# Optimization experiments

Hardware: AMD Instinct MI355X
Metric: run time of the kernel (lower is better)

The kernel has to match this reference:

```python
import jax, jax.numpy as jnp
import numpy as np

B, T, C, H, W = 2, 1, 256, 64, 64
K = 16384  # codebook_size

def setup_inputs() -> dict:
    key = jax.random.key(0)
    k1, k2 = jax.random.split(key)
    x = jax.random.normal(k1, (B, T, C, H, W), dtype=jnp.float32)
    # original init: uniform(-1/K, 1/K); scale is irrelevant for argmin correctness
    codebook = jax.random.uniform(k2, (K, C), dtype=jnp.float32,
                                  minval=-1.0 / K, maxval=1.0 / K)
    return {"x": x, "codebook": codebook}

def reference(x, codebook):
    b, t, c, h, w = x.shape
    # (b,t,c,h,w) -> (b,t,h,w,c) -> (N, c)
    xf = jnp.transpose(x, (0, 1, 3, 4, 2)).reshape(-1, c)
    x_sq = jnp.sum(xf * xf, axis=1, keepdims=True)          # (N, 1)
    e_sq = jnp.sum(codebook * codebook, axis=1)             # (K,)
    d = x_sq + e_sq - 2.0 * jnp.einsum('nd,kd->nk', xf, codebook)  # (N, K)
    indices = jnp.argmin(d, axis=1)
    return indices.reshape(b, t, h, w)
```

## Files before the change

### kernel.cpp

```cpp
#include <hip/hip_runtime.h>
#include <hip/hip_bf16.h>
#include <stdint.h>

constexpr int C    = 256;
constexpr int HW   = 4096;
constexpr int NPIX = 8192;
constexpr int K    = 16384;

constexpr int BM = 128;
constexpr int BN = 256;
constexpr int NB = K / BN;
constexpr float DELTA = 1e-4f;
constexpr unsigned PAIR_CAP = 262144;

typedef __attribute__((ext_vector_type(8))) short short8;
typedef __attribute__((ext_vector_type(4))) float f32x4;
typedef unsigned int u32;
typedef unsigned long long u64;

constexpr size_t OFF_KEYS  = 0;
constexpr size_t OFF_XSQ   = 65536;
constexpr size_t OFF_MHAT  = 98304;
constexpr size_t OFF_CNT   = 131072;
constexpr size_t OFF_PAIRS = 131328;
constexpr size_t OFF_MIN1  = 1179904;
constexpr size_t OFF_K1    = 3277056;
constexpr size_t OFF_MIN2  = 5374208;
constexpr size_t OFF_XT    = 7471360;

static __device__ __forceinline__ unsigned short f2bf(float f) {
    __hip_bfloat16 h = __float2bfloat16(f);
    return *reinterpret_cast<unsigned short*>(&h);
}

__global__ __launch_bounds__(256) void vqprep_kernel(
    const float* __restrict__ x,
    float* __restrict__ xsq, u64* __restrict__ keys,
    unsigned* __restrict__ mhat, unsigned* __restrict__ cnt,
    unsigned short* __restrict__ xt)
{
    __shared__ float lds[64][65];
    const int bid = blockIdx.x;
    const int t   = threadIdx.x;
    if (bid < 32) {
        const int p  = bid * 256 + t;
        const int b  = p >> 12;
        const int hw = p & 4095;
        const float* xp = x + (size_t)b * C * HW + hw;
        float acc = 0.0f;
        #pragma unroll 8
        for (int c = 0; c < C; ++c) {
            const float v = xp[(size_t)c * HW];
            acc = fmaf(v, v, acc);
        }
        xsq[p]  = acc;
        keys[p] = ~0ULL;
        mhat[p] = 0x7F7FFFFFu;
        if (p == 0) *cnt = 0u;
    } else {
        const int bid2 = bid - 32;
        const int hw0 = (bid2 & 63) * 64;
        const int c0  = ((bid2 >> 6) & 3) * 64;
        const int b   = bid2 >> 8;
        #pragma unroll
        for (int i = 0; i < 4; ++i) {
            const int ch  = i * 16 + (t >> 4);
            const int pix = (t & 15) * 4;
            const float4 v = *(const float4*)&x[((size_t)(b * C + c0 + ch)) * HW + hw0 + pix];
            lds[ch][pix + 0] = v.x; lds[ch][pix + 1] = v.y;
            lds[ch][pix + 2] = v.z; lds[ch][pix + 3] = v.w;
        }
        __syncthreads();
        #pragma unroll
        for (int j = 0; j < 4; ++j) {
            const int pix = j * 16 + (t >> 4);
            const int cs  = (t & 15) * 4;
            const u32 lo = (u32)f2bf(lds[cs + 0][pix]) | ((u32)f2bf(lds[cs + 1][pix]) << 16);
            const u32 hi = (u32)f2bf(lds[cs + 2][pix]) | ((u32)f2bf(lds[cs + 3][pix]) << 16);
            const int p = b * HW + hw0 + pix;
            *(uint2*)&xt[(size_t)p * C + c0 + cs] = make_uint2(lo, hi);
        }
    }
}

__global__ __launch_bounds__(256, 2) void vqgemm_kernel(
    const unsigned short* __restrict__ xt, const float* __restrict__ cb,
    float* __restrict__ min1a, unsigned* __restrict__ k1a, float* __restrict__ min2a,
    unsigned* __restrict__ mhat)
{
    __shared__ unsigned short a_lds[128 * 64];
    __shared__ unsigned short b_lds[256 * 64];

    const int t    = threadIdx.x;
    const int lane = t & 63;
    const int wid  = t >> 6;
    const int wr   = wid >> 1;
    const int wc   = wid & 1;
    const int p0 = blockIdx.x * BM;
    const int n0 = blockIdx.y * BN;

    f32x4 acc[4][8];
    #pragma unroll
    for (int i = 0; i < 4; ++i)
        #pragma unroll
        for (int j = 0; j < 8; ++j) acc[i][j] = (f32x4){0.f, 0.f, 0.f, 0.f};

    for (int ks = 0; ks < 4; ++ks) {
        __syncthreads();
        {
            const int r = t >> 1, h = t & 1;
            const char* src = (const char*)xt + (size_t)(p0 + r) * 512 + ks * 128 + h * 64;
            #pragma unroll
            for (int j = 0; j < 4; ++j) {
                const uint4 v = *(const uint4*)(src + j * 16);
                const int s = h * 4 + j;
                *(uint4*)&a_lds[r * 64 + (s ^ (r & 7)) * 8] = v;
            }
        }
        {
            #pragma unroll
            for (int R = 0; R < 4; ++R) {
                const int row = R * 64 + (t >> 2);
                const int seg = t & 3;
                const float* src = cb + (size_t)(n0 + row) * C + ks * 64 + seg * 16;
                u32 w[8];
                #pragma unroll
                for (int j = 0; j < 4; ++j) {
                    const float4 v = *(const float4*)(src + j * 4);
                    w[j * 2 + 0] = (u32)f2bf(v.x) | ((u32)f2bf(v.y) << 16);
                    w[j * 2 + 1] = (u32)f2bf(v.z) | ((u32)f2bf(v.w) << 16);
                }
                const int s0 = seg * 2;
                *(uint4*)&b_lds[row * 64 + ((s0 + 0) ^ (row & 7)) * 8] = make_uint4(w[0], w[1], w[2], w[3]);
                *(uint4*)&b_lds[row * 64 + ((s0 + 1) ^ (row & 7)) * 8] = make_uint4(w[4], w[5], w[6], w[7]);
            }
        }
        __syncthreads();
        #pragma unroll
        for (int kk2 = 0; kk2 < 2; ++kk2) {
            short8 af[4], bfq[8];
            const int sl = kk2 * 4 + (lane >> 4);
            #pragma unroll
            for (int mf = 0; mf < 4; ++mf) {
                const int row = wr * 64 + mf * 16 + (lane & 15);
                af[mf] = *(const short8*)&a_lds[row * 64 + (sl ^ (row & 7)) * 8];
            }
            #pragma unroll
            for (int nf = 0; nf < 8; ++nf) {
                const int row = wc * 128 + nf * 16 + (lane & 15);
                bfq[nf] = *(const short8*)&b_lds[row * 64 + (sl ^ (row & 7)) * 8];
            }
            #pragma unroll
            for (int mf = 0; mf < 4; ++mf)
                #pragma unroll
                for (int nf = 0; nf < 8; ++nf)
                    acc[mf][nf] = __builtin_amdgcn_mfma_f32_16x16x32_bf16(af[mf], bfq[nf], acc[mf][nf], 0, 0, 0);
        }
    }

    __syncthreads();
    u32* tri = (u32*)a_lds;

    #pragma unroll
    for (int mf = 0; mf < 4; ++mf) {
        #pragma unroll
        for (int q = 0; q < 4; ++q) {
            float m1 = 3.4e38f, m2 = 3.4e38f; int kl = 0;
            #pragma unroll
            for (int nf = 0; nf < 8; ++nf) {
                const float v = fmaf(-2.0f, acc[mf][nf][q], 4.0f);
                const int kk = wc * 128 + nf * 16 + (lane & 15);
                if (v < m1) { m2 = m1; m1 = v; kl = kk; }
                else        { m2 = fminf(m2, v); }
            }
            for (int s = 1; s < 16; s <<= 1) {
                const float om1 = __shfl_xor(m1, s);
                const float om2 = __shfl_xor(m2, s);
                const int   okl = __shfl_xor(kl, s);
                if (om1 < m1) { m2 = fminf(m1, om2); m1 = om1; kl = okl; }
                else          { m2 = fminf(om1, m2); }
            }
            if ((lane & 15) == 0) {
                const int pixloc = wr * 64 + mf * 16 + (lane >> 4) * 4 + q;
                const int base = (pixloc * 2 + wc) * 3;
                tri[base + 0] = __float_as_uint(m1);
                tri[base + 1] = (u32)kl;
                tri[base + 2] = __float_as_uint(m2);
            }
        }
    }
    __syncthreads();
    if (t < 128) {
        const int b0 = (t * 2 + 0) * 3, b1 = (t * 2 + 1) * 3;
        float m1 = __uint_as_float(tri[b0 + 0]); u32 kl = tri[b0 + 1];
        float m2 = __uint_as_float(tri[b0 + 2]);
        const float om1 = __uint_as_float(tri[b1 + 0]);
        const u32   okl = tri[b1 + 1];
        const float om2 = __uint_as_float(tri[b1 + 2]);
        if (om1 < m1) { m2 = fminf(m1, om2); m1 = om1; kl = okl; }
        else          { m2 = fminf(om1, m2); }
        const int p = p0 + t;
        const size_t idx = (size_t)p * NB + blockIdx.y;
        min1a[idx] = m1;
        k1a[idx]   = (u32)n0 + kl;
        min2a[idx] = m2;
        atomicMin(&mhat[p], __float_as_uint(m1));
    }
}

__global__ __launch_bounds__(256) void vqflag_kernel(
    const float* __restrict__ min1a, const unsigned* __restrict__ k1a,
    const float* __restrict__ min2a, const unsigned* __restrict__ mhat,
    unsigned* __restrict__ cnt, unsigned* __restrict__ pairs)
{
    const int idx = blockIdx.x * 256 + threadIdx.x;
    if (idx >= NPIX * NB) return;
    const int p  = idx >> 6;
    const int nb = idx & 63;
    const float thresh = __uint_as_float(mhat[p]) + DELTA;
    if (min1a[idx] <= thresh) {
        const unsigned pos = atomicAdd(cnt, 1u);
        if (pos < PAIR_CAP) pairs[pos] = ((unsigned)p << 14) | k1a[idx];
    }
    if (min2a[idx] <= thresh) {
        const unsigned base = atomicAdd(cnt, 256u);
        for (int j = 0; j < 256; ++j)
            if (base + j < PAIR_CAP) pairs[base + j] = ((unsigned)p << 14) | (unsigned)(nb * 256 + j);
    }
}

__global__ __launch_bounds__(256) void vqexact_kernel(
    const float* __restrict__ x, const float* __restrict__ cb,
    const float* __restrict__ xsq, const unsigned* __restrict__ cnt,
    const unsigned* __restrict__ pairs, u64* __restrict__ keys)
{
    const unsigned n = min(*cnt, PAIR_CAP);
    for (unsigned i = blockIdx.x * 256 + threadIdx.x; i < n; i += gridDim.x * 256) {
        const unsigned pair = pairs[i];
        const int p = pair >> 14;
        const int k = pair & 16383;
        const int b = p >> 12;
        const int hw = p & 4095;
        const float* xp = x + (size_t)b * C * HW + hw;
        const float* ep = cb + (size_t)k * C;
        float acc = 0.0f;
        #pragma unroll 4
        for (int c = 0; c < C; ++c)
            acc = fmaf(xp[(size_t)c * HW], ep[c], acc);
        const float d = xsq[p] - 2.0f * acc;
        const u64 key = ((u64)__float_as_uint(d) << 32) | (unsigned)k;
        atomicMin(&keys[p], key);
    }
}

__global__ __launch_bounds__(256) void vqout_kernel(
    const u64* __restrict__ keys, int* __restrict__ out)
{
    const int p = blockIdx.x * 256 + threadIdx.x;
    out[p] = (int)(unsigned)(keys[p] & 0xffffffffu);
}

extern "C" void kernel_launch(void* const* d_in, const int* in_sizes, int n_in,
                              void* d_out, int out_size, void* d_ws, size_t ws_size,
                              hipStream_t stream)
{
    const float* x  = (const float*)d_in[0];
    const float* cb = (const float*)d_in[1];
    int* out = (int*)d_out;
    char* ws = (char*)d_ws;

    u64*      keys  = (u64*)(ws + OFF_KEYS);
    float*    xsq   = (float*)(ws + OFF_XSQ);
    unsigned* mhat  = (unsigned*)(ws + OFF_MHAT);
    unsigned* cnt   = (unsigned*)(ws + OFF_CNT);
    unsigned* pairs = (unsigned*)(ws + OFF_PAIRS);
    float*    min1a = (float*)(ws + OFF_MIN1);
    unsigned* k1a   = (unsigned*)(ws + OFF_K1);
    float*    min2a = (float*)(ws + OFF_MIN2);
    unsigned short* xt = (unsigned short*)(ws + OFF_XT);

    vqprep_kernel<<<544, 256, 0, stream>>>(x, xsq, keys, mhat, cnt, xt);
    vqgemm_kernel<<<dim3(NPIX / BM, K / BN), 256, 0, stream>>>(xt, cb, min1a, k1a, min2a, mhat);
    vqflag_kernel<<<(NPIX * NB) / 256, 256, 0, stream>>>(min1a, k1a, min2a, mhat, cnt, pairs);
    vqexact_kernel<<<1024, 256, 0, stream>>>(x, cb, xsq, cnt, pairs, keys);
    vqout_kernel<<<NPIX / 256, 256, 0, stream>>>(keys, out);
}
```

Baseline: 395.0 us.

## Precast codebook to bf16 once and restructure candidate resolution per pixel

The prep kernel now also converts the whole codebook to bf16 into workspace, so each GEMM block loads bf16 tiles directly instead of converting fp32 on every load. This conversion was previously repeated by all 64 row-blocks. The flag and exact kernels are replaced by a per-pixel resolve kernel that checks single-candidate blocks in exact fp32 inline, and queues only ambiguous whole blocks (by pixel and block index) to a rescan kernel. The rescan kernel evaluates the 256 codes of each queued block with one thread per code and a wave shuffle reduction. The trade-off is an extra 8 MB workspace buffer plus a conversion pass, a serial 64-iteration loop per pixel with uncoalesced fp32 loads, and a smaller queue capacity.

```diff
diff --git a/kernel.cpp b/kernel.cpp
--- a/kernel.cpp
+++ b/kernel.cpp
@@ -11,33 +11,51 @@
 constexpr int BN = 256;
 constexpr int NB = K / BN;
 constexpr float DELTA = 1e-4f;
-constexpr unsigned PAIR_CAP = 262144;
+constexpr unsigned RB_CAP = 32768;
 
 typedef __attribute__((ext_vector_type(8))) short short8;
 typedef __attribute__((ext_vector_type(4))) float f32x4;
 typedef unsigned int u32;
 typedef unsigned long long u64;
 
-constexpr size_t OFF_KEYS  = 0;
-constexpr size_t OFF_XSQ   = 65536;
-constexpr size_t OFF_MHAT  = 98304;
-constexpr size_t OFF_CNT   = 131072;
-constexpr size_t OFF_PAIRS = 131328;
-constexpr size_t OFF_MIN1  = 1179904;
-constexpr size_t OFF_K1    = 3277056;
-constexpr size_t OFF_MIN2  = 5374208;
-constexpr size_t OFF_XT    = 7471360;
+constexpr size_t OFF_KEYS = 0;
+constexpr size_t OFF_XSQ  = 65536;
+constexpr size_t OFF_MHAT = 98304;
+constexpr size_t OFF_RCNT = 131072;
+constexpr size_t OFF_RB   = 135168;
+constexpr size_t OFF_MIN1 = 1048576;
+constexpr size_t OFF_K1   = 3145728;
+constexpr size_t OFF_MIN2 = 5242880;
+constexpr size_t OFF_XT   = 7340032;
+constexpr size_t OFF_CBT  = 11534336;
+constexpr size_t TOTAL_FAST = 19922944;
 
 static __device__ __forceinline__ unsigned short f2bf(float f) {
     __hip_bfloat16 h = __float2bfloat16(f);
     return *reinterpret_cast<unsigned short*>(&h);
 }
 
+static __device__ __forceinline__ float exact_d(
+    const float* __restrict__ x, const float* __restrict__ cb,
+    float xq, int p, int k)
+{
+    const int b  = p >> 12;
+    const int hw = p & 4095;
+    const float* xp = x + (size_t)b * C * HW + hw;
+    const float* ep = cb + (size_t)k * C;
+    float acc = 0.0f;
+    #pragma unroll 4
+    for (int c = 0; c < C; ++c)
+        acc = fmaf(xp[(size_t)c * HW], ep[c], acc);
+    return xq - 2.0f * acc;
+}
+
 __global__ __launch_bounds__(256) void vqprep_kernel(
-    const float* __restrict__ x,
+    const float* __restrict__ x, const float* __restrict__ cb,
     float* __restrict__ xsq, u64* __restrict__ keys,
-    unsigned* __restrict__ mhat, unsigned* __restrict__ cnt,
-    unsigned short* __restrict__ xt)
+    unsigned* __restrict__ mhat, unsigned* __restrict__ rcnt,
+    unsigned short* __restrict__ xt, unsigned short* __restrict__ cbt,
+    int ncbt)
 {
     __shared__ float lds[64][65];
     const int bid = blockIdx.x;
@@ -56,9 +74,19 @@
         xsq[p]  = acc;
         keys[p] = ~0ULL;
         mhat[p] = 0x7F7FFFFFu;
-        if (p == 0) *cnt = 0u;
+        if (p == 0) *rcnt = 0u;
+    } else if (bid < 32 + ncbt) {
+        const size_t idx = (size_t)(bid - 32) * 2048 + (size_t)t * 8;
+        const float4 v0 = *(const float4*)&cb[idx];
+        const float4 v1 = *(const float4*)&cb[idx + 4];
+        uint4 o;
+        o.x = (u32)f2bf(v0.x) | ((u32)f2bf(v0.y) << 16);
+        o.y = (u32)f2bf(v0.z) | ((u32)f2bf(v0.w) << 16);
+        o.z = (u32)f2bf(v1.x) | ((u32)f2bf(v1.y) << 16);
+        o.w = (u32)f2bf(v1.z) | ((u32)f2bf(v1.w) << 16);
+        *(uint4*)&cbt[idx] = o;
     } else {
-        const int bid2 = bid - 32;
+        const int bid2 = bid - 32 - ncbt;
         const int hw0 = (bid2 & 63) * 64;
         const int c0  = ((bid2 >> 6) & 3) * 64;
         const int b   = bid2 >> 8;
@@ -83,8 +111,10 @@
     }
 }
 
+template<bool CBT>
 __global__ __launch_bounds__(256, 2) void vqgemm_kernel(
-    const unsigned short* __restrict__ xt, const float* __restrict__ cb,
+    const unsigned short* __restrict__ xt, const unsigned short* __restrict__ cbt,
+    const float* __restrict__ cb,
     float* __restrict__ min1a, unsigned* __restrict__ k1a, float* __restrict__ min2a,
     unsigned* __restrict__ mhat)
 {
@@ -117,7 +147,19 @@
                 *(uint4*)&a_lds[r * 64 + (s ^ (r & 7)) * 8] = v;
             }
         }
-        {
+        if (CBT) {
+            #pragma unroll
+            for (int R = 0; R < 4; ++R) {
+                const int row = R * 64 + (t >> 2);
+                const int seg = t & 3;
+                const unsigned short* src = cbt + (size_t)(n0 + row) * C + ks * 64 + seg * 16;
+                const uint4 w0 = *(const uint4*)(src);
+                const uint4 w1 = *(const uint4*)(src + 8);
+                const int s0 = seg * 2;
+                *(uint4*)&b_lds[row * 64 + ((s0 + 0) ^ (row & 7)) * 8] = w0;
+                *(uint4*)&b_lds[row * 64 + ((s0 + 1) ^ (row & 7)) * 8] = w1;
+            }
+        } else {
             #pragma unroll
             for (int R = 0; R < 4; ++R) {
                 const int row = R * 64 + (t >> 2);
@@ -208,48 +250,53 @@
     }
 }
 
-__global__ __launch_bounds__(256) void vqflag_kernel(
+__global__ __launch_bounds__(256) void vqresolve_kernel(
+    const float* __restrict__ x, const float* __restrict__ cb,
+    const float* __restrict__ xsq,
     const float* __restrict__ min1a, const unsigned* __restrict__ k1a,
     const float* __restrict__ min2a, const unsigned* __restrict__ mhat,
-    unsigned* __restrict__ cnt, unsigned* __restrict__ pairs)
-{
-    const int idx = blockIdx.x * 256 + threadIdx.x;
-    if (idx >= NPIX * NB) return;
-    const int p  = idx >> 6;
-    const int nb = idx & 63;
+    unsigned* __restrict__ rcnt, unsigned* __restrict__ rb,
+    u64* __restrict__ keys)
+{
+    const int p = blockIdx.x * 256 + threadIdx.x;
     const float thresh = __uint_as_float(mhat[p]) + DELTA;
-    if (min1a[idx] <= thresh) {
-        const unsigned pos = atomicAdd(cnt, 1u);
-        if (pos < PAIR_CAP) pairs[pos] = ((unsigned)p << 14) | k1a[idx];
-    }
-    if (min2a[idx] <= thresh) {
-        const unsigned base = atomicAdd(cnt, 256u);
-        for (int j = 0; j < 256; ++j)
-            if (base + j < PAIR_CAP) pairs[base + j] = ((unsigned)p << 14) | (unsigned)(nb * 256 + j);
-    }
-}
-
-__global__ __launch_bounds__(256) void vqexact_kernel(
+    const float xq = xsq[p];
+    u64 best = ~0ULL;
+    const size_t base = (size_t)p * NB;
+    for (int nb = 0; nb < NB; ++nb) {
+        if (min1a[base + nb] <= thresh) {
+            const int k = (int)k1a[base + nb];
+            const float d = exact_d(x, cb, xq, p, k);
+            const u64 key = ((u64)__float_as_uint(d) << 32) | (u32)k;
+            best = (key < best) ? key : best;
+        }
+        if (min2a[base + nb] <= thresh) {
+            const unsigned pos = atomicAdd(rcnt, 1u);
+            if (pos < RB_CAP) rb[pos] = ((u32)p << 6) | (u32)nb;
+        }
+    }
+    atomicMin(&keys[p], best);
+}
+
+__global__ __launch_bounds__(256) void vqrescan_kernel(
     const float* __restrict__ x, const float* __restrict__ cb,
-    const float* __restrict__ xsq, const unsigned* __restrict__ cnt,
-    const unsigned* __restrict__ pairs, u64* __restrict__ keys)
-{
-    const unsigned n = min(*cnt, PAIR_CAP);
-    for (unsigned i = blockIdx.x * 256 + threadIdx.x; i < n; i += gridDim.x * 256) {
-        const unsigned pair = pairs[i];
-        const int p = pair >> 14;
-        const int k = pair & 16383;
-        const int b = p >> 12;
-        const int hw = p & 4095;
-        const float* xp = x + (size_t)b * C * HW + hw;
-        const float* ep = cb + (size_t)k * C;
-        float acc = 0.0f;
-        #pragma unroll 4
-        for (int c = 0; c < C; ++c)
-            acc = fmaf(xp[(size_t)c * HW], ep[c], acc);
-        const float d = xsq[p] - 2.0f * acc;
-        const u64 key = ((u64)__float_as_uint(d) << 32) | (unsigned)k;
-        atomicMin(&keys[p], key);
+    const float* __restrict__ xsq, const unsigned* __restrict__ rcnt,
+    const unsigned* __restrict__ rb, u64* __restrict__ keys)
+{
+    const unsigned n = min(*rcnt, RB_CAP);
+    for (unsigned i = blockIdx.x; i < n; i += gridDim.x) {
+        const u32 e = rb[i];
+        const int p  = (int)(e >> 6);
+        const int nb = (int)(e & 63u);
+        const int k  = nb * 256 + threadIdx.x;
+        const float d = exact_d(x, cb, xsq[p], p, k);
+        u64 key = ((u64)__float_as_uint(d) << 32) | (u32)k;
+        #pragma unroll
+        for (int s = 1; s < 64; s <<= 1) {
+            const u64 o = __shfl_xor(key, s);
+            key = (o < key) ? o : key;
+        }
+        if ((threadIdx.x & 63) == 0) atomicMin(&keys[p], key);
     }
 }
 
@@ -269,19 +316,26 @@
     int* out = (int*)d_out;
     char* ws = (char*)d_ws;
 
-    u64*      keys  = (u64*)(ws + OFF_KEYS);
-    float*    xsq   = (float*)(ws + OFF_XSQ);
-    unsigned* mhat  = (unsigned*)(ws + OFF_MHAT);
-    unsigned* cnt   = (unsigned*)(ws + OFF_CNT);
-    unsigned* pairs = (unsigned*)(ws + OFF_PAIRS);
+    u64*      keys = (u64*)(ws + OFF_KEYS);
+    float*    xsq  = (float*)(ws + OFF_XSQ);
+    unsigned* mhat = (unsigned*)(ws + OFF_MHAT);
+    unsigned* rcnt = (unsigned*)(ws + OFF_RCNT);
+    unsigned* rb   = (unsigned*)(ws + OFF_RB);
     float*    min1a = (float*)(ws + OFF_MIN1);
     unsigned* k1a   = (unsigned*)(ws + OFF_K1);
     float*    min2a = (float*)(ws + OFF_MIN2);
-    unsigned short* xt = (unsigned short*)(ws + OFF_XT);
-
-    vqprep_kernel<<<544, 256, 0, stream>>>(x, xsq, keys, mhat, cnt, xt);
-    vqgemm_kernel<<<dim3(NPIX / BM, K / BN), 256, 0, stream>>>(xt, cb, min1a, k1a, min2a, mhat);
-    vqflag_kernel<<<(NPIX * NB) / 256, 256, 0, stream>>>(min1a, k1a, min2a, mhat, cnt, pairs);
-    vqexact_kernel<<<1024, 256, 0, stream>>>(x, cb, xsq, cnt, pairs, keys);
+    unsigned short* xt  = (unsigned short*)(ws + OFF_XT);
+    unsigned short* cbt = (unsigned short*)(ws + OFF_CBT);
+
+    const bool fast = (ws_size >= TOTAL_FAST);
+    const int ncbt = fast ? 2048 : 0;
+
+    vqprep_kernel<<<32 + ncbt + 512, 256, 0, stream>>>(x, cb, xsq, keys, mhat, rcnt, xt, cbt, ncbt);
+    if (fast)
+        vqgemm_kernel<true><<<dim3(NPIX / BM, K / BN), 256, 0, stream>>>(xt, cbt, cb, min1a, k1a, min2a, mhat);
+    else
+        vqgemm_kernel<false><<<dim3(NPIX / BM, K / BN), 256, 0, stream>>>(xt, cbt, cb, min1a, k1a, min2a, mhat);
+    vqresolve_kernel<<<NPIX / 256, 256, 0, stream>>>(x, cb, xsq, min1a, k1a, min2a, mhat, rcnt, rb, keys);
+    vqrescan_kernel<<<256, 256, 0, stream>>>(x, cb, xsq, rcnt, rb, keys);
     vqout_kernel<<<NPIX / 256, 256, 0, stream>>>(keys, out);
 }
```

New measurement: 1.024 ms. 2.59x slower.
